# Optimization experiments

Hardware: AMD Instinct MI355X
Metric: run time of the kernel (lower is better)

## Reference

```python
import jax, jax.numpy as jnp
import numpy as np

EMBED = 192
D_INNER = 2 * EMBED          # expand=2
D_STATE = 4                  # low_rank
D_CONV = 4
DT_RANK = (EMBED + 15) // 16 # ceil(192/16) = 12
N_MIX = 2
RANK = 4                     # LowRankProjection rank
B_, H_, W_ = 8, 64, 64


def setup_inputs() -> dict:
    key = jax.random.key(0)
    ks = jax.random.split(key, 16)
    s = lambda *sh: 1.0 / np.sqrt(sh[-1])
    inp = {
        "x": jax.random.normal(ks[0], (B_, EMBED, H_, W_), jnp.float32),
        # stacked per-mixer Mamba params (leading dim N_MIX)
        "in_proj_w": jax.random.normal(ks[1], (N_MIX, 2 * D_INNER, EMBED), jnp.float32) * s(EMBED),
        "conv_w": jax.random.normal(ks[2], (N_MIX, D_INNER, D_CONV), jnp.float32) * s(D_CONV),
        "conv_b": jnp.zeros((N_MIX, D_INNER), jnp.float32),
        "x_proj_w": jax.random.normal(ks[3], (N_MIX, DT_RANK + 2 * D_STATE, D_INNER), jnp.float32) * s(D_INNER),
        "dt_proj_w": jax.random.normal(ks[4], (N_MIX, D_INNER, DT_RANK), jnp.float32) * s(DT_RANK),
        "dt_proj_b": jax.random.uniform(ks[5], (N_MIX, D_INNER), jnp.float32, -4.0, -2.0),
        "A_log": jnp.tile(jnp.log(jnp.arange(1, D_STATE + 1, dtype=jnp.float32))[None, None, :], (N_MIX, D_INNER, 1)),
        "D": jnp.ones((N_MIX, D_INNER), jnp.float32),
        "out_proj_w": jax.random.normal(ks[6], (N_MIX, EMBED, D_INNER), jnp.float32) * s(D_INNER),
        # LowRankProjection
        "U_w": jax.random.normal(ks[7], (RANK, EMBED), jnp.float32) * s(EMBED),
        "V_w": jax.random.normal(ks[8], (EMBED, RANK), jnp.float32) * s(RANK),
        # LayerNorm
        "ln_g": jnp.ones((EMBED,), jnp.float32),
        "ln_b": jnp.zeros((EMBED,), jnp.float32),
    }
    return inp


def _silu(x):
    return x * jax.nn.sigmoid(x)


def _mamba(x, in_proj_w, conv_w, conv_b, x_proj_w, dt_proj_w, dt_proj_b, A_log, D, out_proj_w):
    # x: (B, L, d_model)
    B, L, _ = x.shape
    xz = jnp.einsum("bld,ed->ble", x, in_proj_w)          # (B, L, 2*d_inner)
    xin, z = jnp.split(xz, 2, axis=-1)
    # causal depthwise conv over L
    xt = jnp.transpose(xin, (0, 2, 1))                      # (B, d_inner, L)
    xc = jax.lax.conv_general_dilated(
        xt, conv_w[:, None, :], window_strides=(1,), padding=[(D_CONV - 1, 0)],
        feature_group_count=D_INNER, dimension_numbers=("NCH", "OIH", "NCH"))
    xa = _silu(jnp.transpose(xc + conv_b[None, :, None], (0, 2, 1)))  # (B, L, d_inner)
    x_dbl = jnp.einsum("bld,ed->ble", xa, x_proj_w)         # (B, L, dt_rank+2*d_state)
    dt_lr = x_dbl[..., :DT_RANK]
    Bm = x_dbl[..., DT_RANK:DT_RANK + D_STATE]              # (B, L, d_state)
    Cm = x_dbl[..., DT_RANK + D_STATE:]                     # (B, L, d_state)
    dt = jax.nn.softplus(jnp.einsum("blr,dr->bld", dt_lr, dt_proj_w) + dt_proj_b)  # (B, L, d_inner)
    A = -jnp.exp(A_log)                                     # (d_inner, d_state)
    dA = jnp.exp(dt[..., None] * A)                         # (B, L, d_inner, d_state)
    dBu = dt[..., None] * Bm[:, :, None, :] * xa[..., None]  # (B, L, d_inner, d_state)

    def step(h, inputs):
        dA_i, dBu_i, C_i = inputs                           # (B,d_inner,d_state),(B,d_inner,d_state),(B,d_state)
        h = dA_i * h + dBu_i
        y = jnp.einsum("bds,bs->bd", h, C_i)
        return h, y

    h0 = jnp.zeros((B, D_INNER, D_STATE), x.dtype)
    _, ys = jax.lax.scan(step, h0, (jnp.moveaxis(dA, 1, 0), jnp.moveaxis(dBu, 1, 0), jnp.moveaxis(Cm, 1, 0)))
    y = jnp.moveaxis(ys, 0, 1) + xa * D                     # (B, L, d_inner)
    y = y * _silu(z)
    return jnp.einsum("ble,de->bld", y, out_proj_w)         # (B, L, d_model)


def reference(x, in_proj_w, conv_w, conv_b, x_proj_w, dt_proj_w, dt_proj_b,
              A_log, D, out_proj_w, U_w, V_w, ln_g, ln_b):
    residual = x
    B, C, H, W = x.shape
    h = jnp.transpose(x, (0, 2, 3, 1)).reshape(B, H * W, C)
    for i in range(N_MIX):
        h = _mamba(h, in_proj_w[i], conv_w[i], conv_b[i], x_proj_w[i], dt_proj_w[i],
                   dt_proj_b[i], A_log[i], D[i], out_proj_w[i])
    # low-rank projection
    h = jnp.einsum("blr,dr->bld", jnp.einsum("blc,rc->blr", h, U_w), V_w)
    h = jnp.transpose(h.reshape(B, H, W, C), (0, 3, 1, 2)) + residual
    # LayerNorm over channels
    hc = jnp.transpose(h, (0, 2, 3, 1))
    mu = hc.mean(-1, keepdims=True)
    var = ((hc - mu) ** 2).mean(-1, keepdims=True)
    hc = (hc - mu) * jax.lax.rsqrt(var + 1e-5) * ln_g + ln_b
    return jnp.transpose(hc, (0, 3, 1, 2))
```

## Files before the change

kernel.cpp:

```cpp
#include <hip/hip_runtime.h>
#include <hip/hip_bf16.h>
#include <cstdint>

#define EMBED   192
#define DINNER  384
#define DSTATE  4
#define DCONV   4
#define DTRANK  12
#define NMIX    2
#define RANK    4
#define BB      8
#define LL      4096
#define NBL     (BB*LL)
#define NCHUNK  128
#define CLEN    32

typedef __attribute__((ext_vector_type(8))) short short8;
typedef __attribute__((ext_vector_type(4))) float float4v;

static __device__ __forceinline__ ushort f2b(float f) {
    __hip_bfloat16 h = __float2bfloat16(f);
    return *(ushort*)&h;
}
static __device__ __forceinline__ float b2f(ushort u) {
    __hip_bfloat16 h;
    *(ushort*)&h = u;
    return __bfloat162float(h);
}
static __device__ __forceinline__ float bs2f(short s) {
    ushort u = (ushort)s;
    return b2f(u);
}

#define PREP_N0 294912
#define PREP_N1 147456
#define PREP_N2 24576
#define PREP_N3 24576
#define PREP_N4 3072
__global__ __launch_bounds__(256) void k_prep(const float* __restrict__ in_proj_w,
                                              const float* __restrict__ out_proj_w,
                                              const float* __restrict__ x_proj_w,
                                              const float* __restrict__ dt_proj_w,
                                              const float* __restrict__ conv_w,
                                              ushort* __restrict__ wi,
                                              ushort* __restrict__ wo,
                                              ushort* __restrict__ xpwb,
                                              ushort* __restrict__ dtwpad,
                                              float* __restrict__ cwt) {
    int i = blockIdx.x * 256 + threadIdx.x;
    if (i < PREP_N0) {
        wi[i] = f2b(in_proj_w[i]);
        return;
    }
    i -= PREP_N0;
    if (i < PREP_N1) {
        wo[i] = f2b(out_proj_w[i]);
        return;
    }
    i -= PREP_N1;
    if (i < PREP_N2) {
        int mix = i / (32 * 384);
        int rem = i % (32 * 384);
        int e = rem / 384, k = rem % 384;
        xpwb[i] = (e < 20) ? f2b(x_proj_w[(size_t)mix * 20 * 384 + e * 384 + k]) : (ushort)0;
        return;
    }
    i -= PREP_N2;
    if (i < PREP_N3) {
        int mix = i / (384 * 32);
        int rem = i % (384 * 32);
        int n = rem / 32, r = rem % 32;
        dtwpad[i] = (r < DTRANK) ? f2b(dt_proj_w[(size_t)mix * 384 * DTRANK + n * DTRANK + r])
                                 : (ushort)0;
        return;
    }
    i -= PREP_N3;
    if (i < PREP_N4) {
        int mix = i / (DCONV * DINNER);
        int rem = i % (DCONV * DINNER);
        int k = rem / DINNER, d = rem % DINNER;
        cwt[i] = conv_w[(size_t)mix * DINNER * DCONV + d * DCONV + k];
    }
}

__global__ __launch_bounds__(256) void k_transpose(const float* __restrict__ x,
                                                   ushort* __restrict__ h0b) {
    __shared__ float tile[32][33];
    int b  = blockIdx.z;
    int c0 = blockIdx.y * 32;
    int l0 = blockIdx.x * 32;
    int tx = threadIdx.x;
    int ty = threadIdx.y;
    #pragma unroll
    for (int i = 0; i < 4; i++) {
        int c = c0 + ty + i * 8;
        tile[ty + i * 8][tx] = x[((size_t)b * EMBED + c) * LL + l0 + tx];
    }
    __syncthreads();
    #pragma unroll
    for (int i = 0; i < 4; i++) {
        int l = l0 + ty + i * 8;
        h0b[((size_t)b * LL + l) * EMBED + c0 + tx] = f2b(tile[tx][ty + i * 8]);
    }
}

template<int TN, int WRN>
__global__ __launch_bounds__(256) void k_gemm_bf16(const ushort* __restrict__ A, int lda,
                                                   const ushort* __restrict__ Bw, int ldb,
                                                   float* __restrict__ C, int ldc,
                                                   ushort* __restrict__ Cb, int ldcb,
                                                   int K) {
    constexpr int WRM = 4 / WRN;
    constexpr int WM  = 128 / WRM;
    constexpr int MT  = WM / 16;
    __shared__ ushort As[128][40];
    __shared__ ushort Bs[TN][40];
    int tid  = threadIdx.x;
    int lane = tid & 63;
    int wave = tid >> 6;
    int wmo = (wave / WRN) * WM;
    int wno = (wave % WRN) * 64;
    int m0 = blockIdx.y * 128;
    int n0 = blockIdx.x * TN;

    float4v acc[MT][4];
    #pragma unroll
    for (int i = 0; i < MT; i++)
        #pragma unroll
        for (int j = 0; j < 4; j++)
            acc[i][j] = (float4v){0.f, 0.f, 0.f, 0.f};

    for (int k0 = 0; k0 < K; k0 += 32) {
        #pragma unroll
        for (int i = 0; i < 2; i++) {
            int idx = tid + i * 256;
            int r = idx >> 2, sg = idx & 3;
            *(short8*)&As[r][sg * 8] =
                *(const short8*)(A + (size_t)(m0 + r) * lda + k0 + sg * 8);
        }
        #pragma unroll
        for (int i = 0; i < TN / 64; i++) {
            int idx = tid + i * 256;
            int r = idx >> 2, sg = idx & 3;
            *(short8*)&Bs[r][sg * 8] =
                *(const short8*)(Bw + (size_t)(n0 + r) * ldb + k0 + sg * 8);
        }
        __syncthreads();
        short8 av[MT], bv[4];
        #pragma unroll
        for (int i = 0; i < MT; i++)
            av[i] = *(const short8*)&As[wmo + i * 16 + (lane & 15)][(lane >> 4) * 8];
        #pragma unroll
        for (int j = 0; j < 4; j++)
            bv[j] = *(const short8*)&Bs[wno + j * 16 + (lane & 15)][(lane >> 4) * 8];
        #pragma unroll
        for (int i = 0; i < MT; i++)
            #pragma unroll
            for (int j = 0; j < 4; j++)
                acc[i][j] = __builtin_amdgcn_mfma_f32_16x16x32_bf16(
                    av[i], bv[j], acc[i][j], 0, 0, 0);
        __syncthreads();
    }

    #pragma unroll
    for (int i = 0; i < MT; i++) {
        int rbase = m0 + wmo + i * 16 + (lane >> 4) * 4;
        #pragma unroll
        for (int j = 0; j < 4; j++) {
            int col = n0 + wno + j * 16 + (lane & 15);
            #pragma unroll
            for (int r = 0; r < 4; r++) {
                float v = acc[i][j][r];
                if (C)  C[(size_t)(rbase + r) * ldc + col] = v;
                if (Cb) Cb[(size_t)(rbase + r) * ldcb + col] = f2b(v);
            }
        }
    }
}

__global__ __launch_bounds__(256) void k_conv_silu(const ushort* __restrict__ xz,
                                                   const float* __restrict__ cwt,
                                                   const float* __restrict__ cb,
                                                   ushort* __restrict__ xa) {
    int t   = blockIdx.x * 256 + threadIdx.x;
    int g   = t % 48;
    int blc = t / 48;
    int d0  = g * 8;
    int lc  = blc % (LL / 8);
    int b   = blc / (LL / 8);
    int l0  = lc * 8;

    float wk[4][8], bias[8];
    #pragma unroll
    for (int k = 0; k < 4; k++) {
        float4v wa = *(const float4v*)(cwt + k * DINNER + d0);
        float4v wb = *(const float4v*)(cwt + k * DINNER + d0 + 4);
        #pragma unroll
        for (int j = 0; j < 4; j++) { wk[k][j] = wa[j]; wk[k][j + 4] = wb[j]; }
    }
    {
        float4v ba = *(const float4v*)(cb + d0);
        float4v bb = *(const float4v*)(cb + d0 + 4);
        #pragma unroll
        for (int j = 0; j < 4; j++) { bias[j] = ba[j]; bias[j + 4] = bb[j]; }
    }

    float r0[8] = {}, r1[8] = {}, r2[8] = {};
    const ushort* px = xz + ((size_t)(b * LL + l0)) * 768 + d0;
    if (l0 > 0) {
        short8 v;
        v = *(const short8*)(px - 3 * 768);
        #pragma unroll
        for (int j = 0; j < 8; j++) r0[j] = bs2f(v[j]);
        v = *(const short8*)(px - 2 * 768);
        #pragma unroll
        for (int j = 0; j < 8; j++) r1[j] = bs2f(v[j]);
        v = *(const short8*)(px - 1 * 768);
        #pragma unroll
        for (int j = 0; j < 8; j++) r2[j] = bs2f(v[j]);
    }
    ushort* po = xa + ((size_t)(b * LL + l0)) * DINNER + d0;
    #pragma unroll
    for (int i = 0; i < 8; i++) {
        short8 v = *(const short8*)(px + (size_t)i * 768);
        float cur[8];
        #pragma unroll
        for (int j = 0; j < 8; j++) cur[j] = bs2f(v[j]);
        short8 ov;
        #pragma unroll
        for (int j = 0; j < 8; j++) {
            float a = bias[j] + wk[0][j] * r0[j] + wk[1][j] * r1[j]
                    + wk[2][j] * r2[j] + wk[3][j] * cur[j];
            float sv = a / (1.f + __expf(-a));
            ov[j] = (short)f2b(sv);
        }
        *(short8*)(po + (size_t)i * DINNER) = ov;
        #pragma unroll
        for (int j = 0; j < 8; j++) { r0[j] = r1[j]; r1[j] = r2[j]; r2[j] = cur[j]; }
    }
}

__global__ __launch_bounds__(256) void k_xproj_dt(const ushort* __restrict__ xa,
                                                  const ushort* __restrict__ xpwb,
                                                  const ushort* __restrict__ dtwpad,
                                                  const float* __restrict__ dtb,
                                                  float* __restrict__ xdb32,
                                                  ushort* __restrict__ dtv) {
    __shared__ ushort As[128][40];
    __shared__ ushort Bs[32][40];
    __shared__ ushort Xs[128][40];
    int tid  = threadIdx.x;
    int lane = tid & 63;
    int wave = tid >> 6;
    int m0 = blockIdx.x * 128;
    float4v acc[2][2];
    #pragma unroll
    for (int i = 0; i < 2; i++)
        #pragma unroll
        for (int j = 0; j < 2; j++)
            acc[i][j] = (float4v){0.f, 0.f, 0.f, 0.f};
    for (int k0 = 0; k0 < 384; k0 += 32) {
        #pragma unroll
        for (int i = 0; i < 2; i++) {
            int idx = tid + i * 256;
            int r = idx >> 2, sg = idx & 3;
            *(short8*)&As[r][sg * 8] =
                *(const short8*)(xa + (size_t)(m0 + r) * 384 + k0 + sg * 8);
        }
        if (tid < 128) {
            int r = tid >> 2, sg = tid & 3;
            *(short8*)&Bs[r][sg * 8] =
                *(const short8*)(xpwb + (size_t)r * 384 + k0 + sg * 8);
        }
        __syncthreads();
        short8 av[2], bv[2];
        #pragma unroll
        for (int i = 0; i < 2; i++)
            av[i] = *(const short8*)&As[wave * 32 + i * 16 + (lane & 15)][(lane >> 4) * 8];
        #pragma unroll
        for (int j = 0; j < 2; j++)
            bv[j] = *(const short8*)&Bs[j * 16 + (lane & 15)][(lane >> 4) * 8];
        #pragma unroll
        for (int i = 0; i < 2; i++)
            #pragma unroll
            for (int j = 0; j < 2; j++)
                acc[i][j] = __builtin_amdgcn_mfma_f32_16x16x32_bf16(
                    av[i], bv[j], acc[i][j], 0, 0, 0);
        __syncthreads();
    }
    #pragma unroll
    for (int i = 0; i < 2; i++) {
        int rloc = wave * 32 + i * 16 + (lane >> 4) * 4;
        #pragma unroll
        for (int j = 0; j < 2; j++) {
            int col = j * 16 + (lane & 15);
            #pragma unroll
            for (int r = 0; r < 4; r++) {
                float v = acc[i][j][r];
                xdb32[(size_t)(m0 + rloc + r) * 32 + col] = v;
                Xs[rloc + r][col] = f2b(v);
            }
        }
    }
    __syncthreads();
    int ak = (lane >> 4) * 8;
    #pragma unroll
    for (int rt = 0; rt < 2; rt++) {
        int rowb = wave * 32 + rt * 16;
        short8 av = *(const short8*)&Xs[rowb + (lane & 15)][ak];
        int rbase = m0 + rowb + (lane >> 4) * 4;
        #pragma unroll
        for (int j = 0; j < 24; j++) {
            int col = j * 16 + (lane & 15);
            short8 bv = *(const short8*)(dtwpad + (size_t)col * 32 + ak);
            float4v dacc = (float4v){0.f, 0.f, 0.f, 0.f};
            dacc = __builtin_amdgcn_mfma_f32_16x16x32_bf16(av, bv, dacc, 0, 0, 0);
            float bias = dtb[col];
            #pragma unroll
            for (int r = 0; r < 4; r++) {
                float s = dacc[r] + bias;
                float sp = fmaxf(s, 0.f) + __logf(1.f + __expf(-fabsf(s)));
                dtv[(size_t)(rbase + r) * DINNER + col] = f2b(sp);
            }
        }
    }
}

__global__ __launch_bounds__(384) void k_scan_local(const ushort* __restrict__ xa,
                                                    const float* __restrict__ xdb32,
                                                    const ushort* __restrict__ dtvb,
                                                    const float* __restrict__ A_log,
                                                    float* __restrict__ carryT,
                                                    float* __restrict__ carryH) {
    int d     = threadIdx.x;
    int chunk = blockIdx.x;
    int b     = blockIdx.y;
    __shared__ float rows[CLEN * 32];
    size_t rbase = ((size_t)b * LL + (size_t)chunk * CLEN) * 32;
    for (int i = d; i < CLEN * 32; i += 384) rows[i] = xdb32[rbase + i];
    float As[DSTATE];
    #pragma unroll
    for (int s = 0; s < DSTATE; s++) As[s] = -__expf(A_log[d * DSTATE + s]);
    __syncthreads();
    float h[DSTATE] = {0.f, 0.f, 0.f, 0.f};
    float T = 0.f;
    size_t mbase = (size_t)b * LL + (size_t)chunk * CLEN;
    for (int l = 0; l < CLEN; l++) {
        size_t m = mbase + l;
        float dtvv = b2f(dtvb[m * DINNER + d]);
        float xav  = b2f(xa[m * DINNER + d]);
        float du   = dtvv * xav;
        T += dtvv;
        const float* row = &rows[l * 32];
        #pragma unroll
        for (int s = 0; s < DSTATE; s++) {
            float da = __expf(dtvv * As[s]);
            h[s] = da * h[s] + du * row[DTRANK + s];
        }
    }
    size_t cb = ((size_t)chunk * BB + b);
    carryT[cb * 384 + d] = T;
    float4v hv = {h[0], h[1], h[2], h[3]};
    *(float4v*)(carryH + cb * 1536 + d * 4) = hv;
}

__global__ __launch_bounds__(256) void k_scan_combine(const float* __restrict__ carryT,
                                                      const float* __restrict__ carryH,
                                                      const float* __restrict__ A_log,
                                                      float* __restrict__ carryI) {
    int c   = blockIdx.x * 256 + threadIdx.x;
    int b   = c / 1536;
    int rem = c - b * 1536;
    int d   = rem >> 2;
    float As = -__expf(A_log[rem]);
    float hrun = 0.f;
    for (int k = 0; k < NCHUNK; k++) {
        size_t o = (size_t)k * BB + b;
        float T  = carryT[o * 384 + d];
        float Hk = carryH[o * 1536 + rem];
        carryI[o * 1536 + rem] = hrun;
        hrun = __expf(As * T) * hrun + Hk;
    }
}

__global__ __launch_bounds__(384) void k_scan_final(const ushort* __restrict__ xa,
                                                    const ushort* __restrict__ xz,
                                                    const float* __restrict__ xdb32,
                                                    const ushort* __restrict__ dtvb,
                                                    const float* __restrict__ A_log,
                                                    const float* __restrict__ Dp,
                                                    const float* __restrict__ carryI,
                                                    ushort* __restrict__ y) {
    int d     = threadIdx.x;
    int chunk = blockIdx.x;
    int b     = blockIdx.y;
    __shared__ float rows[CLEN * 32];
    size_t rbase = ((size_t)b * LL + (size_t)chunk * CLEN) * 32;
    for (int i = d; i < CLEN * 32; i += 384) rows[i] = xdb32[rbase + i];
    float As[DSTATE];
    #pragma unroll
    for (int s = 0; s < DSTATE; s++) As[s] = -__expf(A_log[d * DSTATE + s]);
    float Dd = Dp[d];
    float4v hv = *(const float4v*)(carryI + ((size_t)chunk * BB + b) * 1536 + d * 4);
    float h[DSTATE];
    #pragma unroll
    for (int s = 0; s < DSTATE; s++) h[s] = hv[s];
    __syncthreads();
    size_t mbase = (size_t)b * LL + (size_t)chunk * CLEN;
    for (int l = 0; l < CLEN; l++) {
        size_t m = mbase + l;
        float dtvv = b2f(dtvb[m * DINNER + d]);
        float xav  = b2f(xa[m * DINNER + d]);
        float du   = dtvv * xav;
        const float* row = &rows[l * 32];
        float yv = 0.f;
        #pragma unroll
        for (int s = 0; s < DSTATE; s++) {
            float da = __expf(dtvv * As[s]);
            h[s] = da * h[s] + du * row[DTRANK + s];
            yv  += h[s] * row[DTRANK + DSTATE + s];
        }
        yv += xav * Dd;
        float zv = b2f(xz[m * 768 + DINNER + d]);
        yv *= zv / (1.f + __expf(-zv));
        y[m * DINNER + d] = f2b(yv);
    }
}

__global__ __launch_bounds__(256) void k_tail(const ushort* __restrict__ h1b,
                                              const ushort* __restrict__ h0b,
                                              const float* __restrict__ U,
                                              const float* __restrict__ V,
                                              const float* __restrict__ g,
                                              const float* __restrict__ be,
                                              float* __restrict__ out) {
    __shared__ float tile[EMBED * 65];
    int tid  = threadIdx.x;
    int lane = tid & 63;
    int wave = tid >> 6;
    int b  = blockIdx.y;
    int l0 = blockIdx.x * 64;
    for (int t = 0; t < 16; t++) {
        int lloc = wave * 16 + t;
        size_t m = (size_t)b * LL + l0 + lloc;
        float hv[3];
        #pragma unroll
        for (int i = 0; i < 3; i++) hv[i] = b2f(h1b[m * EMBED + lane + 64 * i]);
        float r[RANK];
        #pragma unroll
        for (int j = 0; j < RANK; j++) {
            float p = 0.f;
            #pragma unroll
            for (int i = 0; i < 3; i++) p += hv[i] * U[j * EMBED + lane + 64 * i];
            #pragma unroll
            for (int off = 1; off < 64; off <<= 1) p += __shfl_xor(p, off);
            r[j] = p;
        }
        float u[3], s1 = 0.f, s2 = 0.f;
        #pragma unroll
        for (int i = 0; i < 3; i++) {
            int c = lane + 64 * i;
            float v = r[0] * V[c * 4 + 0] + r[1] * V[c * 4 + 1]
                    + r[2] * V[c * 4 + 2] + r[3] * V[c * 4 + 3];
            u[i] = v + b2f(h0b[m * EMBED + c]);
            s1 += u[i];
            s2 += u[i] * u[i];
        }
        #pragma unroll
        for (int off = 1; off < 64; off <<= 1) {
            s1 += __shfl_xor(s1, off);
            s2 += __shfl_xor(s2, off);
        }
        float mean = s1 * (1.f / EMBED);
        float var  = s2 * (1.f / EMBED) - mean * mean;
        float inv  = rsqrtf(var + 1e-5f);
        #pragma unroll
        for (int i = 0; i < 3; i++) {
            int c = lane + 64 * i;
            tile[c * 65 + lloc] = (u[i] - mean) * inv * g[c] + be[c];
        }
    }
    __syncthreads();
    for (int i = tid; i < EMBED * 64; i += 256) {
        int c = i >> 6, l = i & 63;
        out[((size_t)(b * EMBED + c)) * LL + l0 + l] = tile[c * 65 + l];
    }
}

extern "C" void kernel_launch(void* const* d_in, const int* in_sizes, int n_in,
                              void* d_out, int out_size, void* d_ws, size_t ws_size,
                              hipStream_t stream) {
    const float* x          = (const float*)d_in[0];
    const float* in_proj_w  = (const float*)d_in[1];
    const float* conv_w     = (const float*)d_in[2];
    const float* conv_b     = (const float*)d_in[3];
    const float* x_proj_w   = (const float*)d_in[4];
    const float* dt_proj_w  = (const float*)d_in[5];
    const float* dt_proj_b  = (const float*)d_in[6];
    const float* A_log      = (const float*)d_in[7];
    const float* Dp         = (const float*)d_in[8];
    const float* out_proj_w = (const float*)d_in[9];
    const float* U_w        = (const float*)d_in[10];
    const float* V_w        = (const float*)d_in[11];
    const float* ln_g       = (const float*)d_in[12];
    const float* ln_b       = (const float*)d_in[13];
    float* out = (float*)d_out;

    float* ws    = (float*)d_ws;
    float* xdb32 = ws;
    float* carryT = xdb32 + (size_t)NBL * 32;
    float* carryH = carryT + (size_t)NCHUNK * BB * DINNER;
    float* carryI = carryH + (size_t)NCHUNK * BB * DINNER * DSTATE;
    ushort* dtv    = (ushort*)(carryI + (size_t)NCHUNK * BB * DINNER * DSTATE);
    ushort* xz16   = dtv    + (size_t)NBL * DINNER;
    ushort* xa16   = xz16   + (size_t)NBL * 768;
    ushort* yb     = xa16   + (size_t)NBL * DINNER;
    ushort* h0b    = yb     + (size_t)NBL * DINNER;
    ushort* h1b    = h0b    + (size_t)NBL * EMBED;
    ushort* wi     = h1b    + (size_t)NBL * EMBED;
    ushort* wo     = wi     + (size_t)NMIX * 768 * EMBED;
    ushort* xpwb   = wo     + (size_t)NMIX * EMBED * DINNER;
    ushort* dtwpad = xpwb   + (size_t)NMIX * 32 * 384;
    float*  cwt    = (float*)(dtwpad + (size_t)NMIX * 384 * 32);

    k_prep<<<(PREP_N0 + PREP_N1 + PREP_N2 + PREP_N3 + PREP_N4) / 256, 256, 0, stream>>>(
        in_proj_w, out_proj_w, x_proj_w, dt_proj_w, conv_w, wi, wo, xpwb, dtwpad, cwt);

    k_transpose<<<dim3(LL / 32, EMBED / 32, BB), dim3(32, 8), 0, stream>>>(x, h0b);

    const ushort* hinb = h0b;
    for (int mix = 0; mix < NMIX; mix++) {
        const float* Alg = A_log + (size_t)mix * DINNER * DSTATE;

        k_gemm_bf16<128, 2><<<dim3(768 / 128, NBL / 128), 256, 0, stream>>>(
            hinb, EMBED, wi + (size_t)mix * 768 * EMBED, EMBED,
            (float*)nullptr, 0, xz16, 768, EMBED);
        k_conv_silu<<<(NBL / 8 * 48) / 256, 256, 0, stream>>>(
            xz16, cwt + (size_t)mix * DCONV * DINNER, conv_b + mix * DINNER, xa16);
        k_xproj_dt<<<NBL / 128, 256, 0, stream>>>(
            xa16, xpwb + (size_t)mix * 32 * 384, dtwpad + (size_t)mix * 384 * 32,
            dt_proj_b + mix * DINNER, xdb32, dtv);
        k_scan_local<<<dim3(NCHUNK, BB), 384, 0, stream>>>(
            xa16, xdb32, dtv, Alg, carryT, carryH);
        k_scan_combine<<<(BB * DINNER * DSTATE) / 256, 256, 0, stream>>>(
            carryT, carryH, Alg, carryI);
        k_scan_final<<<dim3(NCHUNK, BB), 384, 0, stream>>>(
            xa16, xz16, xdb32, dtv, Alg, Dp + mix * DINNER, carryI, yb);
        k_gemm_bf16<64, 1><<<dim3(EMBED / 64, NBL / 128), 256, 0, stream>>>(
            yb, DINNER, wo + (size_t)mix * EMBED * DINNER, DINNER,
            (float*)nullptr, 0, h1b, EMBED, DINNER);
        hinb = h1b;
    }

    k_tail<<<dim3(LL / 64, BB), 256, 0, stream>>>(h1b, h0b, U_w, V_w, ln_g, ln_b, out);
}
```

Baseline: 437.4 us.

## Recompute dt projection and softplus inside scan kernels instead of materializing dtv

Removes the dt projection MFMA and the bf16 dtv buffer (NBL x 384) from the x_proj kernel. Each scan thread now keeps its 12 dt weights in fp32 registers and recomputes the softplus of the rank-12 dot product per timestep from the shared-memory row. This drops a large global write plus two reads of dtv per mixer. The cost is that dt is computed twice (local and final scan), adding ALU and transcendental work and register pressure to the scan kernels.

```diff
diff --git a/kernel.cpp b/kernel.cpp
--- a/kernel.cpp
+++ b/kernel.cpp
@@ -35,7 +35,7 @@
 #define PREP_N0 294912
 #define PREP_N1 147456
 #define PREP_N2 24576
-#define PREP_N3 24576
+#define PREP_N3 9216
 #define PREP_N4 3072
 __global__ __launch_bounds__(256) void k_prep(const float* __restrict__ in_proj_w,
                                               const float* __restrict__ out_proj_w,
@@ -45,7 +45,7 @@
                                               ushort* __restrict__ wi,
                                               ushort* __restrict__ wo,
                                               ushort* __restrict__ xpwb,
-                                              ushort* __restrict__ dtwpad,
+                                              float* __restrict__ dtwT,
                                               float* __restrict__ cwt) {
     int i = blockIdx.x * 256 + threadIdx.x;
     if (i < PREP_N0) {
@@ -67,11 +67,10 @@
     }
     i -= PREP_N2;
     if (i < PREP_N3) {
-        int mix = i / (384 * 32);
-        int rem = i % (384 * 32);
-        int n = rem / 32, r = rem % 32;
-        dtwpad[i] = (r < DTRANK) ? f2b(dt_proj_w[(size_t)mix * 384 * DTRANK + n * DTRANK + r])
-                                 : (ushort)0;
+        int mix = i / (DTRANK * 384);
+        int rem = i % (DTRANK * 384);
+        int r = rem / 384, d = rem % 384;
+        dtwT[i] = dt_proj_w[(size_t)mix * 384 * DTRANK + d * DTRANK + r];
         return;
     }
     i -= PREP_N3;
@@ -240,15 +239,11 @@
     }
 }
 
-__global__ __launch_bounds__(256) void k_xproj_dt(const ushort* __restrict__ xa,
-                                                  const ushort* __restrict__ xpwb,
-                                                  const ushort* __restrict__ dtwpad,
-                                                  const float* __restrict__ dtb,
-                                                  float* __restrict__ xdb32,
-                                                  ushort* __restrict__ dtv) {
+__global__ __launch_bounds__(256) void k_xproj_mfma(const ushort* __restrict__ xa,
+                                                    const ushort* __restrict__ xpwb,
+                                                    float* __restrict__ xdb32) {
     __shared__ ushort As[128][40];
     __shared__ ushort Bs[32][40];
-    __shared__ ushort Xs[128][40];
     int tid  = threadIdx.x;
     int lane = tid & 63;
     int wave = tid >> 6;
@@ -290,45 +285,30 @@
     }
     #pragma unroll
     for (int i = 0; i < 2; i++) {
-        int rloc = wave * 32 + i * 16 + (lane >> 4) * 4;
+        int rbase = m0 + wave * 32 + i * 16 + (lane >> 4) * 4;
         #pragma unroll
         for (int j = 0; j < 2; j++) {
             int col = j * 16 + (lane & 15);
             #pragma unroll
-            for (int r = 0; r < 4; r++) {
-                float v = acc[i][j][r];
-                xdb32[(size_t)(m0 + rloc + r) * 32 + col] = v;
-                Xs[rloc + r][col] = f2b(v);
-            }
-        }
-    }
-    __syncthreads();
-    int ak = (lane >> 4) * 8;
-    #pragma unroll
-    for (int rt = 0; rt < 2; rt++) {
-        int rowb = wave * 32 + rt * 16;
-        short8 av = *(const short8*)&Xs[rowb + (lane & 15)][ak];
-        int rbase = m0 + rowb + (lane >> 4) * 4;
-        #pragma unroll
-        for (int j = 0; j < 24; j++) {
-            int col = j * 16 + (lane & 15);
-            short8 bv = *(const short8*)(dtwpad + (size_t)col * 32 + ak);
-            float4v dacc = (float4v){0.f, 0.f, 0.f, 0.f};
-            dacc = __builtin_amdgcn_mfma_f32_16x16x32_bf16(av, bv, dacc, 0, 0, 0);
-            float bias = dtb[col];
-            #pragma unroll
-            for (int r = 0; r < 4; r++) {
-                float s = dacc[r] + bias;
-                float sp = fmaxf(s, 0.f) + __logf(1.f + __expf(-fabsf(s)));
-                dtv[(size_t)(rbase + r) * DINNER + col] = f2b(sp);
-            }
-        }
-    }
+            for (int r = 0; r < 4; r++)
+                xdb32[(size_t)(rbase + r) * 32 + col] = acc[i][j][r];
+        }
+    }
+}
+
+static __device__ __forceinline__ float dt_inline(const float* __restrict__ row,
+                                                  const float* __restrict__ w,
+                                                  float bias) {
+    float s = bias;
+    #pragma unroll
+    for (int r = 0; r < DTRANK; r++) s += row[r] * w[r];
+    return fmaxf(s, 0.f) + __logf(1.f + __expf(-fabsf(s)));
 }
 
 __global__ __launch_bounds__(384) void k_scan_local(const ushort* __restrict__ xa,
                                                     const float* __restrict__ xdb32,
-                                                    const ushort* __restrict__ dtvb,
+                                                    const float* __restrict__ dtwT,
+                                                    const float* __restrict__ dtb,
                                                     const float* __restrict__ A_log,
                                                     float* __restrict__ carryT,
                                                     float* __restrict__ carryH) {
@@ -338,6 +318,10 @@
     __shared__ float rows[CLEN * 32];
     size_t rbase = ((size_t)b * LL + (size_t)chunk * CLEN) * 32;
     for (int i = d; i < CLEN * 32; i += 384) rows[i] = xdb32[rbase + i];
+    float w[DTRANK];
+    #pragma unroll
+    for (int r = 0; r < DTRANK; r++) w[r] = dtwT[r * 384 + d];
+    float bias = dtb[d];
     float As[DSTATE];
     #pragma unroll
     for (int s = 0; s < DSTATE; s++) As[s] = -__expf(A_log[d * DSTATE + s]);
@@ -347,11 +331,11 @@
     size_t mbase = (size_t)b * LL + (size_t)chunk * CLEN;
     for (int l = 0; l < CLEN; l++) {
         size_t m = mbase + l;
-        float dtvv = b2f(dtvb[m * DINNER + d]);
+        const float* row = &rows[l * 32];
+        float dtvv = dt_inline(row, w, bias);
         float xav  = b2f(xa[m * DINNER + d]);
         float du   = dtvv * xav;
         T += dtvv;
-        const float* row = &rows[l * 32];
         #pragma unroll
         for (int s = 0; s < DSTATE; s++) {
             float da = __expf(dtvv * As[s]);
@@ -386,7 +370,8 @@
 __global__ __launch_bounds__(384) void k_scan_final(const ushort* __restrict__ xa,
                                                     const ushort* __restrict__ xz,
                                                     const float* __restrict__ xdb32,
-                                                    const ushort* __restrict__ dtvb,
+                                                    const float* __restrict__ dtwT,
+                                                    const float* __restrict__ dtb,
                                                     const float* __restrict__ A_log,
                                                     const float* __restrict__ Dp,
                                                     const float* __restrict__ carryI,
@@ -397,6 +382,10 @@
     __shared__ float rows[CLEN * 32];
     size_t rbase = ((size_t)b * LL + (size_t)chunk * CLEN) * 32;
     for (int i = d; i < CLEN * 32; i += 384) rows[i] = xdb32[rbase + i];
+    float w[DTRANK];
+    #pragma unroll
+    for (int r = 0; r < DTRANK; r++) w[r] = dtwT[r * 384 + d];
+    float bias = dtb[d];
     float As[DSTATE];
     #pragma unroll
     for (int s = 0; s < DSTATE; s++) As[s] = -__expf(A_log[d * DSTATE + s]);
@@ -409,10 +398,10 @@
     size_t mbase = (size_t)b * LL + (size_t)chunk * CLEN;
     for (int l = 0; l < CLEN; l++) {
         size_t m = mbase + l;
-        float dtvv = b2f(dtvb[m * DINNER + d]);
+        const float* row = &rows[l * 32];
+        float dtvv = dt_inline(row, w, bias);
         float xav  = b2f(xa[m * DINNER + d]);
         float du   = dtvv * xav;
-        const float* row = &rows[l * 32];
         float yv = 0.f;
         #pragma unroll
         for (int s = 0; s < DSTATE; s++) {
@@ -511,8 +500,7 @@
     float* carryT = xdb32 + (size_t)NBL * 32;
     float* carryH = carryT + (size_t)NCHUNK * BB * DINNER;
     float* carryI = carryH + (size_t)NCHUNK * BB * DINNER * DSTATE;
-    ushort* dtv    = (ushort*)(carryI + (size_t)NCHUNK * BB * DINNER * DSTATE);
-    ushort* xz16   = dtv    + (size_t)NBL * DINNER;
+    ushort* xz16   = (ushort*)(carryI + (size_t)NCHUNK * BB * DINNER * DSTATE);
     ushort* xa16   = xz16   + (size_t)NBL * 768;
     ushort* yb     = xa16   + (size_t)NBL * DINNER;
     ushort* h0b    = yb     + (size_t)NBL * DINNER;
@@ -520,32 +508,33 @@
     ushort* wi     = h1b    + (size_t)NBL * EMBED;
     ushort* wo     = wi     + (size_t)NMIX * 768 * EMBED;
     ushort* xpwb   = wo     + (size_t)NMIX * EMBED * DINNER;
-    ushort* dtwpad = xpwb   + (size_t)NMIX * 32 * 384;
-    float*  cwt    = (float*)(dtwpad + (size_t)NMIX * 384 * 32);
+    float*  dtwT   = (float*)(xpwb + (size_t)NMIX * 32 * 384);
+    float*  cwt    = dtwT + (size_t)NMIX * DTRANK * 384;
 
     k_prep<<<(PREP_N0 + PREP_N1 + PREP_N2 + PREP_N3 + PREP_N4) / 256, 256, 0, stream>>>(
-        in_proj_w, out_proj_w, x_proj_w, dt_proj_w, conv_w, wi, wo, xpwb, dtwpad, cwt);
+        in_proj_w, out_proj_w, x_proj_w, dt_proj_w, conv_w, wi, wo, xpwb, dtwT, cwt);
 
     k_transpose<<<dim3(LL / 32, EMBED / 32, BB), dim3(32, 8), 0, stream>>>(x, h0b);
 
     const ushort* hinb = h0b;
     for (int mix = 0; mix < NMIX; mix++) {
-        const float* Alg = A_log + (size_t)mix * DINNER * DSTATE;
+        const float* Alg  = A_log + (size_t)mix * DINNER * DSTATE;
+        const float* dtwm = dtwT + (size_t)mix * DTRANK * 384;
+        const float* dtbm = dt_proj_b + mix * DINNER;
 
         k_gemm_bf16<128, 2><<<dim3(768 / 128, NBL / 128), 256, 0, stream>>>(
             hinb, EMBED, wi + (size_t)mix * 768 * EMBED, EMBED,
             (float*)nullptr, 0, xz16, 768, EMBED);
         k_conv_silu<<<(NBL / 8 * 48) / 256, 256, 0, stream>>>(
             xz16, cwt + (size_t)mix * DCONV * DINNER, conv_b + mix * DINNER, xa16);
-        k_xproj_dt<<<NBL / 128, 256, 0, stream>>>(
-            xa16, xpwb + (size_t)mix * 32 * 384, dtwpad + (size_t)mix * 384 * 32,
-            dt_proj_b + mix * DINNER, xdb32, dtv);
+        k_xproj_mfma<<<NBL / 128, 256, 0, stream>>>(
+            xa16, xpwb + (size_t)mix * 32 * 384, xdb32);
         k_scan_local<<<dim3(NCHUNK, BB), 384, 0, stream>>>(
-            xa16, xdb32, dtv, Alg, carryT, carryH);
+            xa16, xdb32, dtwm, dtbm, Alg, carryT, carryH);
         k_scan_combine<<<(BB * DINNER * DSTATE) / 256, 256, 0, stream>>>(
             carryT, carryH, Alg, carryI);
         k_scan_final<<<dim3(NCHUNK, BB), 384, 0, stream>>>(
-            xa16, xz16, xdb32, dtv, Alg, Dp + mix * DINNER, carryI, yb);
+            xa16, xz16, xdb32, dtwm, dtbm, Alg, Dp + mix * DINNER, carryI, yb);
         k_gemm_bf16<64, 1><<<dim3(EMBED / 64, NBL / 128), 256, 0, stream>>>(
             yb, DINNER, wo + (size_t)mix * EMBED * DINNER, DINNER,
             (float*)nullptr, 0, h1b, EMBED, DINNER);
```

Measured after the change: 427.6 us. -2.3%, faster.
